# Kernel optimization log

Measured on AMD Instinct MI355X. Metric: run time of the kernel, lower is better.

The kernel has to match this reference:

```python
import jax, jax.numpy as jnp
import numpy as np

TEMPERATURE = 8.0  # sqrt(d_head=64)

def setup_inputs() -> dict:
    key = jax.random.key(0)
    kq, kk, kv = jax.random.split(key, 3)
    shape = (2, 16, 2048, 64)  # [B, H, S, D]
    q = jax.random.normal(kq, shape, dtype=jnp.float32)
    k = jax.random.normal(kk, shape, dtype=jnp.float32)
    v = jax.random.normal(kv, shape, dtype=jnp.float32)
    return {"q": q, "k": k, "v": v}

def reference(q, k, v):
    # attn = softmax((q / temperature) @ k^T) ; dropout is identity in eval
    scores = jnp.einsum('bhqd,bhkd->bhqk', q / TEMPERATURE, k)  # [B,H,S,S]
    attn = jax.nn.softmax(scores, axis=-1)
    out = jnp.einsum('bhqk,bhkd->bhqd', attn, v)  # [B,H,S,D]
    return out
```

## Files before the change

kernel.cpp:

```cpp
#include <hip/hip_runtime.h>
#include <hip/hip_bf16.h>

typedef __bf16 bf16_t;
typedef bf16_t bf16x4 __attribute__((ext_vector_type(4)));
typedef bf16_t bf16x8 __attribute__((ext_vector_type(8)));
typedef float f32x4 __attribute__((ext_vector_type(4)));

#define S_LEN 2048
#define HD 64
#define NT 32
#define BHN 32
#define QSCALE 0.18033688f

__device__ __forceinline__ void gload16(const bf16_t* g, void* l) {
    __builtin_amdgcn_global_load_lds(
        (const __attribute__((address_space(1))) void*)g,
        (__attribute__((address_space(3))) void*)l, 16, 0, 0);
}

__global__ __launch_bounds__(256)
void prep_kv(const float* __restrict__ kg, const float* __restrict__ vg,
             bf16_t* __restrict__ kb, bf16_t* __restrict__ vtb) {
    __shared__ bf16_t Vl[64 * 68];
    const int tid = threadIdx.x;
    const int kt0 = blockIdx.x * 64;
    const int bh  = blockIdx.y;
    const size_t gbase = (size_t)bh * S_LEN * HD;
    #pragma unroll
    for (int j = 0; j < 4; ++j) {
        int idx = j * 256 + tid;
        int key = idx >> 4;
        int d0  = (idx & 15) * 4;
        const f32x4 k4 = *(const f32x4*)(kg + gbase + (size_t)(kt0 + key) * HD + d0);
        const f32x4 v4 = *(const f32x4*)(vg + gbase + (size_t)(kt0 + key) * HD + d0);
        bf16x4 kbv, vbv;
        #pragma unroll
        for (int e = 0; e < 4; ++e) { kbv[e] = (bf16_t)k4[e]; vbv[e] = (bf16_t)v4[e]; }
        *(bf16x4*)(kb + gbase + (size_t)(kt0 + key) * HD + d0) = kbv;
        *(bf16x4*)&Vl[key * 68 + d0] = vbv;
    }
    __syncthreads();
    const int d   = tid >> 2;
    const int q16 = tid & 3;
    const int kp  = q16 >> 1, h = q16 & 1;
    bf16_t* orow = vtb + (size_t)bh * HD * S_LEN + (size_t)d * S_LEN + kt0;
    #pragma unroll
    for (int gg = 0; gg < 4; ++gg) {
        bf16x4 o;
        #pragma unroll
        for (int r = 0; r < 4; ++r) o[r] = Vl[(q16 * 16 + gg * 4 + r) * 68 + d];
        *(bf16x4*)(orow + kp * 32 + gg * 8 + h * 4) = o;
    }
}

__global__ __launch_bounds__(256, 2)
void attn_fwd_bf16(const float* __restrict__ qg, const bf16_t* __restrict__ kb,
                   const bf16_t* __restrict__ vtb, float* __restrict__ og) {
    __shared__ __align__(16) char lds[32768];

    const int tid  = threadIdx.x;
    const int wave = tid >> 6;
    const int lane = tid & 63;
    const int g    = lane >> 4;
    const int ln   = lane & 15;

    const int fid  = blockIdx.x;
    const int bid2 = (fid & 7) * 64 + (fid >> 3);
    const int bh   = bid2 >> 4;
    const int qt   = bid2 & 15;
    const int qrow0 = qt * 128 + wave * 32;
    const size_t base = (size_t)bh * S_LEN * HD;

    bf16x8 qf[2][2];
    #pragma unroll
    for (int qg2 = 0; qg2 < 2; ++qg2) {
        const float* qp = qg + base + (size_t)(qrow0 + qg2 * 16 + ln) * HD;
        #pragma unroll
        for (int c = 0; c < 2; ++c)
            #pragma unroll
            for (int i = 0; i < 8; ++i)
                qf[qg2][c][i] = (bf16_t)(qp[c * 32 + g * 8 + i] * QSCALE);
    }
    asm volatile("s_waitcnt vmcnt(0)" ::: "memory");

    bf16x8 ones;
    #pragma unroll
    for (int i = 0; i < 8; ++i) ones[i] = (bf16_t)1.0f;

    const int r0 = tid >> 3, s0 = tid & 7, r1 = r0 + 32;
    const bf16_t* kpl = kb + base;
    const bf16_t* vpl = vtb + base;
    const bf16_t* ksA = kpl + r0 * HD + (s0 ^ (r0 & 7)) * 8;
    const bf16_t* ksB = kpl + r1 * HD + (s0 ^ (r1 & 7)) * 8;
    const bf16_t* vsA = vpl + (size_t)r0 * S_LEN + (s0 ^ (r0 & 7)) * 8;
    const bf16_t* vsB = vpl + (size_t)r1 * S_LEN + (s0 ^ (r1 & 7)) * 8;
    char* ldb = lds + tid * 16;

#define STAGE(kt, b) do { \
        gload16(ksA + (size_t)(kt) * 4096, ldb + (b) * 8192); \
        gload16(ksB + (size_t)(kt) * 4096, ldb + (b) * 8192 + 4096); \
        gload16(vsA + (kt) * 64, ldb + 16384 + (b) * 8192); \
        gload16(vsB + (kt) * 64, ldb + 16384 + (b) * 8192 + 4096); \
    } while (0)

    int kof[4][2], voff[4][2];
    #pragma unroll
    for (int kt2 = 0; kt2 < 4; ++kt2)
        #pragma unroll
        for (int c = 0; c < 2; ++c)
            kof[kt2][c] = (kt2 * 16 + ln) * 128 + (((c << 2) + g) ^ (ln & 7)) * 16;
    #pragma unroll
    for (int t = 0; t < 4; ++t)
        #pragma unroll
        for (int kp = 0; kp < 2; ++kp)
            voff[t][kp] = 16384 + (t * 16 + ln) * 128 + (((kp << 2) + g) ^ (ln & 7)) * 16;

    f32x4 acc[2][4];
    f32x4 accl[2];
    #pragma unroll
    for (int qg2 = 0; qg2 < 2; ++qg2) {
        accl[qg2] = f32x4{0.f, 0.f, 0.f, 0.f};
        #pragma unroll
        for (int t = 0; t < 4; ++t) acc[qg2][t] = f32x4{0.f, 0.f, 0.f, 0.f};
    }

    STAGE(0, 0);

    for (int kt = 0; kt < NT; ++kt) {
        asm volatile("s_waitcnt vmcnt(0)" ::: "memory");
        asm volatile("s_barrier" ::: "memory");
        if (kt + 1 < NT) STAGE(kt + 1, (kt + 1) & 1);
        const char* kbr = lds + (kt & 1) * 8192;
        const char* vbr = kbr;

        f32x4 sv01[2][2];
        #pragma unroll
        for (int kt2 = 0; kt2 < 2; ++kt2) {
            const bf16x8 kf0 = *(const bf16x8*)(kbr + kof[kt2][0]);
            const bf16x8 kf1 = *(const bf16x8*)(kbr + kof[kt2][1]);
            #pragma unroll
            for (int qg2 = 0; qg2 < 2; ++qg2) {
                f32x4 s = f32x4{0.f, 0.f, 0.f, 0.f};
                s = __builtin_amdgcn_mfma_f32_16x16x32_bf16(kf0, qf[qg2][0], s, 0, 0, 0);
                s = __builtin_amdgcn_mfma_f32_16x16x32_bf16(kf1, qf[qg2][1], s, 0, 0, 0);
                sv01[kt2][qg2] = s;
            }
        }

        bf16x8 pa0[2];
        #pragma unroll
        for (int qg2 = 0; qg2 < 2; ++qg2)
            #pragma unroll
            for (int i = 0; i < 8; ++i)
                pa0[qg2][i] = (bf16_t)__builtin_amdgcn_exp2f(sv01[i >> 2][qg2][i & 3]);

        f32x4 sv23[2][2];
        #pragma unroll
        for (int kt2 = 0; kt2 < 2; ++kt2) {
            const bf16x8 kf0 = *(const bf16x8*)(kbr + kof[2 + kt2][0]);
            const bf16x8 kf1 = *(const bf16x8*)(kbr + kof[2 + kt2][1]);
            #pragma unroll
            for (int qg2 = 0; qg2 < 2; ++qg2) {
                f32x4 s = f32x4{0.f, 0.f, 0.f, 0.f};
                s = __builtin_amdgcn_mfma_f32_16x16x32_bf16(kf0, qf[qg2][0], s, 0, 0, 0);
                s = __builtin_amdgcn_mfma_f32_16x16x32_bf16(kf1, qf[qg2][1], s, 0, 0, 0);
                sv23[kt2][qg2] = s;
            }
        }

        #pragma unroll
        for (int t = 0; t < 4; ++t) {
            const bf16x8 vf0 = *(const bf16x8*)(vbr + voff[t][0]);
            #pragma unroll
            for (int qg2 = 0; qg2 < 2; ++qg2)
                acc[qg2][t] = __builtin_amdgcn_mfma_f32_16x16x32_bf16(pa0[qg2], vf0, acc[qg2][t], 0, 0, 0);
        }

        bf16x8 pa1[2];
        #pragma unroll
        for (int qg2 = 0; qg2 < 2; ++qg2)
            #pragma unroll
            for (int i = 0; i < 8; ++i)
                pa1[qg2][i] = (bf16_t)__builtin_amdgcn_exp2f(sv23[i >> 2][qg2][i & 3]);

        #pragma unroll
        for (int t = 0; t < 4; ++t) {
            const bf16x8 vf1 = *(const bf16x8*)(vbr + voff[t][1]);
            #pragma unroll
            for (int qg2 = 0; qg2 < 2; ++qg2)
                acc[qg2][t] = __builtin_amdgcn_mfma_f32_16x16x32_bf16(pa1[qg2], vf1, acc[qg2][t], 0, 0, 0);
        }

        #pragma unroll
        for (int qg2 = 0; qg2 < 2; ++qg2) {
            accl[qg2] = __builtin_amdgcn_mfma_f32_16x16x32_bf16(pa0[qg2], ones, accl[qg2], 0, 0, 0);
            accl[qg2] = __builtin_amdgcn_mfma_f32_16x16x32_bf16(pa1[qg2], ones, accl[qg2], 0, 0, 0);
        }
    }
#undef STAGE

    #pragma unroll
    for (int qg2 = 0; qg2 < 2; ++qg2) {
        float* ob = og + base + (size_t)(qrow0 + qg2 * 16) * HD;
        float il[4];
        #pragma unroll
        for (int r = 0; r < 4; ++r) il[r] = 1.f / accl[qg2][r];
        #pragma unroll
        for (int t = 0; t < 4; ++t)
            #pragma unroll
            for (int r = 0; r < 4; ++r)
                ob[(size_t)(4 * g + r) * HD + t * 16 + ln] = acc[qg2][t][r] * il[r];
    }
}

#define LDP 72
__global__ __launch_bounds__(256, 2)
void attn_fwd_fallback(const float* __restrict__ qg, const float* __restrict__ kg,
                       const float* __restrict__ vg, float* __restrict__ og) {
    __shared__ __align__(16) bf16_t Kl[64 * LDP];
    __shared__ __align__(16) bf16_t Vt[HD * LDP];
    const int tid = threadIdx.x, wave = tid >> 6, lane = tid & 63;
    const int g = lane >> 4, ln = lane & 15;
    const int bh = blockIdx.y, qrow0 = blockIdx.x * 64 + wave * 16;
    const size_t base = (size_t)bh * S_LEN * HD;
    bf16x8 qf[2];
    {
        const float* qp = qg + base + (size_t)(qrow0 + ln) * HD;
        #pragma unroll
        for (int c = 0; c < 2; ++c)
            #pragma unroll
            for (int i = 0; i < 8; ++i) qf[c][i] = (bf16_t)(qp[c * 32 + g * 8 + i] * 0.125f);
    }
    f32x4 acc[4];
    #pragma unroll
    for (int t = 0; t < 4; ++t) acc[t] = f32x4{0.f, 0.f, 0.f, 0.f};
    float m_run = -3e38f, l_run = 0.f;
    const float* kbase = kg + base;
    const float* vbase = vg + base;
    const int vkb = (tid & 15) * 4, vdb = (tid >> 4) * 4;
    for (int kt = 0; kt < NT; ++kt) {
        __syncthreads();
        #pragma unroll
        for (int j = 0; j < 4; ++j) {
            int idx = j * 256 + tid, key = idx >> 4, d0 = (idx & 15) * 4;
            const f32x4 k4 = *(const f32x4*)(kbase + (size_t)(kt * 64 + key) * HD + d0);
            bf16x4 kbv;
            #pragma unroll
            for (int e = 0; e < 4; ++e) kbv[e] = (bf16_t)k4[e];
            *(bf16x4*)&Kl[key * LDP + d0] = kbv;
        }
        {
            f32x4 v4[4];
            #pragma unroll
            for (int e = 0; e < 4; ++e)
                v4[e] = *(const f32x4*)(vbase + (size_t)(kt * 64 + vkb + e) * HD + vdb);
            #pragma unroll
            for (int j = 0; j < 4; ++j) {
                bf16x4 vb;
                #pragma unroll
                for (int e = 0; e < 4; ++e) vb[e] = (bf16_t)v4[e][j];
                *(bf16x4*)&Vt[(vdb + j) * LDP + vkb] = vb;
            }
        }
        __syncthreads();
        float p[4][4];
        float mx = -3e38f;
        #pragma unroll
        for (int kt2 = 0; kt2 < 4; ++kt2) {
            f32x4 sx = f32x4{0.f, 0.f, 0.f, 0.f};
            #pragma unroll
            for (int c = 0; c < 2; ++c) {
                const bf16x8 kf = *(const bf16x8*)&Kl[(kt2 * 16 + ln) * LDP + c * 32 + g * 8];
                sx = __builtin_amdgcn_mfma_f32_16x16x32_bf16(kf, qf[c], sx, 0, 0, 0);
            }
            #pragma unroll
            for (int rr = 0; rr < 4; ++rr) { p[kt2][rr] = sx[rr]; mx = fmaxf(mx, sx[rr]); }
        }
        mx = fmaxf(mx, __shfl_xor(mx, 16, 64));
        mx = fmaxf(mx, __shfl_xor(mx, 32, 64));
        const float mnew = fmaxf(m_run, mx);
        const float scale = __expf(m_run - mnew);
        m_run = mnew;
        float rs = 0.f;
        #pragma unroll
        for (int kt2 = 0; kt2 < 4; ++kt2)
            #pragma unroll
            for (int rr = 0; rr < 4; ++rr) {
                const float e = __expf(p[kt2][rr] - mnew);
                p[kt2][rr] = e; rs += e;
            }
        rs += __shfl_xor(rs, 16, 64);
        rs += __shfl_xor(rs, 32, 64);
        l_run = l_run * scale + rs;
        float sc[4];
        #pragma unroll
        for (int rr = 0; rr < 4; ++rr) sc[rr] = __shfl(scale, 4 * g + rr, 64);
        #pragma unroll
        for (int t = 0; t < 4; ++t)
            #pragma unroll
            for (int rr = 0; rr < 4; ++rr) acc[t][rr] *= sc[rr];
        bf16x8 pa[2];
        #pragma unroll
        for (int kp = 0; kp < 2; ++kp)
            #pragma unroll
            for (int i = 0; i < 8; ++i) pa[kp][i] = (bf16_t)p[2 * kp + (i >> 2)][i & 3];
        #pragma unroll
        for (int t = 0; t < 4; ++t)
            #pragma unroll
            for (int kp = 0; kp < 2; ++kp) {
                const bf16_t* vrow = &Vt[(t * 16 + ln) * LDP + 32 * kp + 4 * g];
                const bf16x4 lo = *(const bf16x4*)(vrow);
                const bf16x4 hi = *(const bf16x4*)(vrow + 16);
                bf16x8 vf;
                #pragma unroll
                for (int e = 0; e < 4; ++e) { vf[e] = lo[e]; vf[4 + e] = hi[e]; }
                acc[t] = __builtin_amdgcn_mfma_f32_16x16x32_bf16(pa[kp], vf, acc[t], 0, 0, 0);
            }
    }
    const float invl = 1.f / l_run;
    float il[4];
    #pragma unroll
    for (int rr = 0; rr < 4; ++rr) il[rr] = __shfl(invl, 4 * g + rr, 64);
    float* ob = og + base + (size_t)qrow0 * HD;
    #pragma unroll
    for (int t = 0; t < 4; ++t)
        #pragma unroll
        for (int rr = 0; rr < 4; ++rr)
            ob[(size_t)(4 * g + rr) * HD + t * 16 + ln] = acc[t][rr] * il[rr];
}

extern "C" void kernel_launch(void* const* d_in, const int* in_sizes, int n_in,
                              void* d_out, int out_size, void* d_ws, size_t ws_size,
                              hipStream_t stream) {
    const float* q = (const float*)d_in[0];
    const float* k = (const float*)d_in[1];
    const float* v = (const float*)d_in[2];
    float* out = (float*)d_out;
    const int bh = in_sizes[0] / (S_LEN * HD);
    const size_t plane = (size_t)bh * S_LEN * HD;
    const size_t need  = 2 * plane * sizeof(bf16_t);

    if (bh == BHN && ws_size >= need) {
        bf16_t* kb  = (bf16_t*)d_ws;
        bf16_t* vtb = kb + plane;
        prep_kv<<<dim3(NT, bh), 256, 0, stream>>>(k, v, kb, vtb);
        attn_fwd_bf16<<<dim3(bh * 16), 256, 0, stream>>>(q, kb, vtb, out);
    } else {
        attn_fwd_fallback<<<dim3(S_LEN / 64, bh), 256, 0, stream>>>(q, k, v, out);
    }
}
```

Before: 53.08 us.

## Split KV sequence across two blocks per query tile and reduce partials

Adds a split-K (flash-decoding style) mode where each query tile is processed by two blocks, each covering half the key range. The blocks write unnormalized partial outputs and row sums to workspace, and a separate reduce kernel sums the halves and normalizes. The aim is to double the grid from 512 to 1024 blocks and raise the occupancy target to 4 blocks per SM to fill the GPU better. In exchange it adds a third launch plus extra global traffic for the fp32 partials. The softmax has no max subtraction, so summing the halves directly is valid.

```diff
diff --git a/kernel.cpp b/kernel.cpp
--- a/kernel.cpp
+++ b/kernel.cpp
@@ -53,9 +53,11 @@
     }
 }
 
-__global__ __launch_bounds__(256, 2)
+__global__ __launch_bounds__(256, 4)
 void attn_fwd_bf16(const float* __restrict__ qg, const bf16_t* __restrict__ kb,
-                   const bf16_t* __restrict__ vtb, float* __restrict__ og) {
+                   const bf16_t* __restrict__ vtb, float* __restrict__ og,
+                   float* __restrict__ opart, float* __restrict__ lpart,
+                   const int nsplit) {
     __shared__ __align__(16) char lds[32768];
 
     const int tid  = threadIdx.x;
@@ -64,12 +66,17 @@
     const int g    = lane >> 4;
     const int ln   = lane & 15;
 
-    const int fid  = blockIdx.x;
-    const int bid2 = (fid & 7) * 64 + (fid >> 3);
+    const int fid    = blockIdx.x;
+    const int nblk8  = (gridDim.x >> 3);
+    int bid2 = (fid & 7) * nblk8 + (fid >> 3);
+    int half = 0;
+    if (nsplit == 2) { half = bid2 & 1; bid2 >>= 1; }
     const int bh   = bid2 >> 4;
     const int qt   = bid2 & 15;
     const int qrow0 = qt * 128 + wave * 32;
     const size_t base = (size_t)bh * S_LEN * HD;
+    const int kt0 = half * (NT / 2);
+    const int ktn = NT / nsplit;
 
     bf16x8 qf[2][2];
     #pragma unroll
@@ -124,12 +131,12 @@
         for (int t = 0; t < 4; ++t) acc[qg2][t] = f32x4{0.f, 0.f, 0.f, 0.f};
     }
 
-    STAGE(0, 0);
-
-    for (int kt = 0; kt < NT; ++kt) {
+    STAGE(kt0, 0);
+
+    for (int kt = 0; kt < ktn; ++kt) {
         asm volatile("s_waitcnt vmcnt(0)" ::: "memory");
         asm volatile("s_barrier" ::: "memory");
-        if (kt + 1 < NT) STAGE(kt + 1, (kt + 1) & 1);
+        if (kt + 1 < ktn) STAGE(kt0 + kt + 1, (kt + 1) & 1);
         const char* kbr = lds + (kt & 1) * 8192;
         const char* vbr = kbr;
 
@@ -199,18 +206,53 @@
     }
 #undef STAGE
 
-    #pragma unroll
-    for (int qg2 = 0; qg2 < 2; ++qg2) {
-        float* ob = og + base + (size_t)(qrow0 + qg2 * 16) * HD;
-        float il[4];
-        #pragma unroll
-        for (int r = 0; r < 4; ++r) il[r] = 1.f / accl[qg2][r];
-        #pragma unroll
-        for (int t = 0; t < 4; ++t)
-            #pragma unroll
-            for (int r = 0; r < 4; ++r)
-                ob[(size_t)(4 * g + r) * HD + t * 16 + ln] = acc[qg2][t][r] * il[r];
-    }
+    if (nsplit == 1) {
+        #pragma unroll
+        for (int qg2 = 0; qg2 < 2; ++qg2) {
+            float* ob = og + base + (size_t)(qrow0 + qg2 * 16) * HD;
+            float il[4];
+            #pragma unroll
+            for (int r = 0; r < 4; ++r) il[r] = 1.f / accl[qg2][r];
+            #pragma unroll
+            for (int t = 0; t < 4; ++t)
+                #pragma unroll
+                for (int r = 0; r < 4; ++r)
+                    ob[(size_t)(4 * g + r) * HD + t * 16 + ln] = acc[qg2][t][r] * il[r];
+        }
+    } else {
+        const size_t TOT = (size_t)BHN * S_LEN * HD;
+        #pragma unroll
+        for (int qg2 = 0; qg2 < 2; ++qg2) {
+            float* ob = opart + (size_t)half * TOT + base + (size_t)(qrow0 + qg2 * 16) * HD;
+            #pragma unroll
+            for (int t = 0; t < 4; ++t)
+                #pragma unroll
+                for (int r = 0; r < 4; ++r)
+                    ob[(size_t)(4 * g + r) * HD + t * 16 + ln] = acc[qg2][t][r];
+            if (ln == 0) {
+                float* lb = lpart + (size_t)half * BHN * S_LEN + (size_t)bh * S_LEN
+                          + qrow0 + qg2 * 16;
+                #pragma unroll
+                for (int r = 0; r < 4; ++r) lb[4 * g + r] = accl[qg2][r];
+            }
+        }
+    }
+}
+
+__global__ __launch_bounds__(256)
+void reduce_halves(const float* __restrict__ opart, const float* __restrict__ lpart,
+                   float* __restrict__ og) {
+    const size_t TOT = (size_t)BHN * S_LEN * HD;
+    const size_t idx = (size_t)blockIdx.x * 256 + threadIdx.x;
+    const size_t e = idx * 4;
+    const size_t row = idx >> 4;
+    const f32x4 a = *(const f32x4*)(opart + e);
+    const f32x4 b = *(const f32x4*)(opart + TOT + e);
+    const float il = 1.f / (lpart[row] + lpart[(size_t)BHN * S_LEN + row]);
+    f32x4 o;
+    #pragma unroll
+    for (int j = 0; j < 4; ++j) o[j] = (a[j] + b[j]) * il;
+    *(f32x4*)(og + e) = o;
 }
 
 #define LDP 72
@@ -338,13 +380,23 @@
     float* out = (float*)d_out;
     const int bh = in_sizes[0] / (S_LEN * HD);
     const size_t plane = (size_t)bh * S_LEN * HD;
-    const size_t need  = 2 * plane * sizeof(bf16_t);
-
-    if (bh == BHN && ws_size >= need) {
+    const size_t kvbytes = 2 * plane * sizeof(bf16_t);
+    const size_t need_full = kvbytes + 2 * plane * sizeof(float)
+                           + 2 * (size_t)bh * S_LEN * sizeof(float);
+
+    if (bh == BHN && ws_size >= need_full) {
+        bf16_t* kb    = (bf16_t*)d_ws;
+        bf16_t* vtb   = kb + plane;
+        float*  opart = (float*)(vtb + plane);
+        float*  lpart = opart + 2 * plane;
+        prep_kv<<<dim3(NT, bh), 256, 0, stream>>>(k, v, kb, vtb);
+        attn_fwd_bf16<<<dim3(bh * 16 * 2), 256, 0, stream>>>(q, kb, vtb, out, opart, lpart, 2);
+        reduce_halves<<<dim3((unsigned)(plane / 4 / 256)), 256, 0, stream>>>(opart, lpart, out);
+    } else if (bh == BHN && ws_size >= kvbytes) {
         bf16_t* kb  = (bf16_t*)d_ws;
         bf16_t* vtb = kb + plane;
         prep_kv<<<dim3(NT, bh), 256, 0, stream>>>(k, v, kb, vtb);
-        attn_fwd_bf16<<<dim3(bh * 16), 256, 0, stream>>>(q, kb, vtb, out);
+        attn_fwd_bf16<<<dim3(bh * 16), 256, 0, stream>>>(q, kb, vtb, out, nullptr, nullptr, 1);
     } else {
         attn_fwd_fallback<<<dim3(S_LEN / 64, bh), 256, 0, stream>>>(q, k, v, out);
     }
```

New measurement: 60.92 us. 14.8% more time.
